# Optimization experiments

Hardware: AMD Instinct MI355X
Metric: run time of the kernel (lower is better)

Reference implementation:

```python
import jax, jax.numpy as jnp
import numpy as np

NBINS = 256


def _equalize_hist(img):
    # img: [H, W] float32 with values in [0, 255]; replicates cv2.equalizeHist
    vals = jnp.clip(img.astype(jnp.int32), 0, NBINS - 1).reshape(-1)
    hist = jnp.zeros((NBINS,), jnp.float32).at[vals].add(1.0)
    cdf = jnp.cumsum(hist)
    total = jnp.float32(vals.shape[0])
    # cdf value at the first nonzero bin (cv2 maps that bin to 0)
    cdf_min = cdf[jnp.argmax(hist > 0)]
    scale = (NBINS - 1.0) / jnp.maximum(total - cdf_min, 1.0)
    lut = jnp.clip(jnp.round((cdf - cdf_min) * scale), 0.0, 255.0)
    return lut[vals].reshape(img.shape) / 255.0


def setup_inputs() -> dict:
    key = jax.random.key(0)
    k1, _ = jax.random.split(key)
    # uint8-like pixel values stored as float32, shape [B, 1, H, W]
    image = jnp.floor(jax.random.uniform(k1, (64, 1, 1024, 1024), jnp.float32) * 256.0)
    image = jnp.clip(image, 0.0, 255.0)
    kernel = jnp.array([[[[0.0, 1.0, 0.0], [1.0, -4.0, 1.0], [0.0, 1.0, 0.0]]]], jnp.float32)
    return {"image": image, "kernel": kernel}


def reference(image, kernel):
    # per-image histogram equalization (channels == 1, as in the torch loop)
    eq = jax.vmap(_equalize_hist)(image[:, 0, :, :])[:, None, :, :]  # [B,1,H,W]
    laplace = jax.lax.conv_general_dilated(
        eq, kernel,
        window_strides=(1, 1), padding=((1, 1), (1, 1)),
        dimension_numbers=("NCHW", "OIHW", "NCHW"))
    # torch.var defaults to unbiased (ddof=1) over all elements
    return jnp.var(laplace, ddof=1)
```

## Files before the change

kernel.cpp:

```cpp
#include <hip/hip_runtime.h>

#define W 1024
#define H 1024
#define NIMG 64
#define NBINS 256
#define NPIX (W * H)
#define NTOT ((long long)NIMG * NPIX)
#define NSLOT 256
#define RPW 8

typedef float f32x4 __attribute__((ext_vector_type(4)));

#define WS_HIST 0
#define WS_LUTP 65536
#define WS_ACC  81920
#define WS_SMALL 86016
#define WS_U8   (128 * 1024)
#define WS_FAST (WS_U8 + (size_t)NIMG * NPIX)

template <bool WRITE_U8>
__global__ __launch_bounds__(256) void hist_kernel(const float* __restrict__ img,
                                                   unsigned int* __restrict__ ghist,
                                                   unsigned char* __restrict__ u8img) {
    __shared__ unsigned int lh[NBINS];
    const int b = blockIdx.y;
    lh[threadIdx.x] = 0u;
    __syncthreads();
    const size_t base = (size_t)b * NPIX;
    const f32x4* p = (const f32x4*)(img + base);
    uchar4* q8 = (uchar4*)(u8img + base);
    const int nvec = NPIX / 4;
    const int stride = gridDim.x * 256;
    for (int i = blockIdx.x * 256 + threadIdx.x; i < nvec; i += stride) {
        f32x4 v = __builtin_nontemporal_load(&p[i]);
        int i0 = min(max((int)v[0], 0), 255);
        int i1 = min(max((int)v[1], 0), 255);
        int i2 = min(max((int)v[2], 0), 255);
        int i3 = min(max((int)v[3], 0), 255);
        atomicAdd(&lh[i0], 1u);
        atomicAdd(&lh[i1], 1u);
        atomicAdd(&lh[i2], 1u);
        atomicAdd(&lh[i3], 1u);
        if (WRITE_U8) {
            q8[i] = make_uchar4((unsigned char)i0, (unsigned char)i1,
                                (unsigned char)i2, (unsigned char)i3);
        }
    }
    __syncthreads();
    unsigned int c = lh[threadIdx.x];
    if (c) atomicAdd(&ghist[b * NBINS + threadIdx.x], c);
}

__global__ __launch_bounds__(256) void lut_kernel(const unsigned int* __restrict__ ghist,
                                                  unsigned int* __restrict__ lutp) {
    __shared__ float cdf[NBINS];
    __shared__ unsigned char lut8[NBINS];
    __shared__ float s_min;
    const int b = blockIdx.x;
    const int t = threadIdx.x;
    cdf[t] = (float)ghist[b * NBINS + t];
    __syncthreads();
    for (int off = 1; off < NBINS; off <<= 1) {
        float add = (t >= off) ? cdf[t - off] : 0.0f;
        __syncthreads();
        cdf[t] += add;
        __syncthreads();
    }
    if (t == 0) {
        float m = 0.0f;
        for (int i = 0; i < NBINS; ++i) {
            if (cdf[i] > 0.0f) { m = cdf[i]; break; }
        }
        s_min = m;
    }
    __syncthreads();
    const float scale = 255.0f / fmaxf((float)NPIX - s_min, 1.0f);
    float L = fminf(fmaxf(rintf((cdf[t] - s_min) * scale), 0.0f), 255.0f);
    lut8[t] = (unsigned char)L;
    __syncthreads();
    if (t < 64) {
        unsigned int w = (unsigned int)lut8[4 * t] |
                         ((unsigned int)lut8[4 * t + 1] << 8) |
                         ((unsigned int)lut8[4 * t + 2] << 16) |
                         ((unsigned int)lut8[4 * t + 3] << 24);
        lutp[b * 64 + t] = w;
    }
}

template <bool USE_U8>
__global__ __launch_bounds__(256) void lap_kernel(const float* __restrict__ img,
                                                  const unsigned char* __restrict__ u8img,
                                                  const unsigned int* __restrict__ lutp,
                                                  unsigned long long* __restrict__ acc) {
    const int b = blockIdx.y;
    const int lane = threadIdx.x & 63;
    const int wv = threadIdx.x >> 6;
    const int y0 = blockIdx.x * (RPW * 4) + wv * RPW;
    const int col0 = lane * 16;
    const unsigned int lutw = lutp[b * 64 + lane];
    const size_t base = (size_t)b * NPIX;
    const unsigned char* rowp8 = u8img + base + col0;
    const float* rowpf = img + base + col0;

    unsigned int p_[4], c_[4], n_[4];

    auto load_raw = [&](int gy, unsigned int raw[4]) {
        if ((unsigned)gy < (unsigned)H) {
            if (USE_U8) {
                uint4 r = *(const uint4*)(rowp8 + (size_t)gy * W);
                raw[0] = r.x; raw[1] = r.y; raw[2] = r.z; raw[3] = r.w;
            } else {
                const f32x4* fp = (const f32x4*)(rowpf + (size_t)gy * W);
#pragma unroll
                for (int k = 0; k < 4; ++k) {
                    f32x4 v = fp[k];
                    unsigned int w = (unsigned int)min(max((int)v[0], 0), 255);
                    w |= (unsigned int)min(max((int)v[1], 0), 255) << 8;
                    w |= (unsigned int)min(max((int)v[2], 0), 255) << 16;
                    w |= (unsigned int)min(max((int)v[3], 0), 255) << 24;
                    raw[k] = w;
                }
            }
        } else {
            raw[0] = raw[1] = raw[2] = raw[3] = 0u;
        }
    };
    auto gather_row = [&](const unsigned int raw[4], bool valid, unsigned int ew[4]) {
#pragma unroll
        for (int k = 0; k < 4; ++k) {
            unsigned int out = 0u;
#pragma unroll
            for (int j = 0; j < 4; ++j) {
                int v = (int)((raw[k] >> (8 * j)) & 0xFFu);
                unsigned int e = (unsigned int)__builtin_amdgcn_ds_bpermute(v & 0xFC, (int)lutw);
                out |= ((e >> ((v & 3) << 3)) & 0xFFu) << (8 * j);
            }
            ew[k] = valid ? out : 0u;
        }
    };

    unsigned int rawB[4], rawC[4];
    load_raw(y0 - 1, rawB);
    gather_row(rawB, y0 - 1 >= 0, p_);
    load_raw(y0, rawB);
    gather_row(rawB, true, c_);
    load_raw(y0 + 1, rawB);

    int s = 0, q = 0;
#pragma unroll
    for (int rr = 0; rr < RPW; ++rr) {
        const int gy = y0 + rr;
        if (rr + 1 < RPW) load_raw(gy + 2, rawC);
        gather_row(rawB, gy + 1 < H, n_);

        unsigned int t3 = (unsigned int)__shfl_up((int)c_[3], 1, 64);
        const int lw = (lane == 0) ? 0 : (int)(t3 >> 24);
        unsigned int t0 = (unsigned int)__shfl_down((int)c_[0], 1, 64);
        const int rw = (lane == 63) ? 0 : (int)(t0 & 0xFFu);

#pragma unroll
        for (int p = 0; p < 16; ++p) {
            const int k = p >> 2, sh = (p & 3) << 3;
            const int c = (int)((c_[k] >> sh) & 0xFFu);
            const int u = (int)((p_[k] >> sh) & 0xFFu);
            const int d = (int)((n_[k] >> sh) & 0xFFu);
            const int l = (p == 0) ? lw
                        : (int)((c_[(p - 1) >> 2] >> (((p - 1) & 3) << 3)) & 0xFFu);
            const int r = (p == 15) ? rw
                        : (int)((c_[(p + 1) >> 2] >> (((p + 1) & 3) << 3)) & 0xFFu);
            const int lap = u + d + l + r - 4 * c;
            s += lap;
            q += lap * lap;
        }
#pragma unroll
        for (int k = 0; k < 4; ++k) { p_[k] = c_[k]; c_[k] = n_[k]; rawB[k] = rawC[k]; }
    }

    long long S = s, Q = q;
    for (int off = 32; off > 0; off >>= 1) {
        S += __shfl_down(S, off, 64);
        Q += __shfl_down(Q, off, 64);
    }
    if (lane == 0) {
        const int wid = (blockIdx.x + blockIdx.y * gridDim.x) * 4 + wv;
        const int slot = wid & (NSLOT - 1);
        atomicAdd(&acc[2 * slot], (unsigned long long)S);
        atomicAdd(&acc[2 * slot + 1], (unsigned long long)Q);
    }
}

__global__ __launch_bounds__(256) void finalize_kernel(const unsigned long long* __restrict__ acc,
                                                       float* __restrict__ out) {
    const int t = threadIdx.x;
    long long S = (long long)acc[2 * t];
    long long Q = (long long)acc[2 * t + 1];
    for (int off = 32; off > 0; off >>= 1) {
        S += __shfl_down(S, off, 64);
        Q += __shfl_down(Q, off, 64);
    }
    __shared__ long long ss[4], sq[4];
    const int wave = t >> 6, lane = t & 63;
    if (lane == 0) { ss[wave] = S; sq[wave] = Q; }
    __syncthreads();
    if (t == 0) {
        long long St = ss[0] + ss[1] + ss[2] + ss[3];
        long long Qt = sq[0] + sq[1] + sq[2] + sq[3];
        const double N = (double)NTOT;
        double Sr = (double)St / 255.0;
        double Qr = (double)Qt / 65025.0;
        out[0] = (float)((Qr - Sr * Sr / N) / (N - 1.0));
    }
}

extern "C" void kernel_launch(void* const* d_in, const int* in_sizes, int n_in,
                              void* d_out, int out_size, void* d_ws, size_t ws_size,
                              hipStream_t stream) {
    const float* img = (const float*)d_in[0];
    float* out = (float*)d_out;

    unsigned int* ghist     = (unsigned int*)((char*)d_ws + WS_HIST);
    unsigned int* lutp      = (unsigned int*)((char*)d_ws + WS_LUTP);
    unsigned long long* acc = (unsigned long long*)((char*)d_ws + WS_ACC);
    unsigned char* u8img    = (unsigned char*)((char*)d_ws + WS_U8);

    const bool fast = (ws_size >= WS_FAST);

    hipMemsetAsync(d_ws, 0, WS_SMALL, stream);

    dim3 hgrid(64, NIMG);
    if (fast) hist_kernel<true><<<hgrid, 256, 0, stream>>>(img, ghist, u8img);
    else      hist_kernel<false><<<hgrid, 256, 0, stream>>>(img, ghist, u8img);

    lut_kernel<<<NIMG, NBINS, 0, stream>>>(ghist, lutp);

    dim3 lgrid(H / (RPW * 4), NIMG);
    if (fast) lap_kernel<true><<<lgrid, 256, 0, stream>>>(img, u8img, lutp, acc);
    else      lap_kernel<false><<<lgrid, 256, 0, stream>>>(img, u8img, lutp, acc);

    finalize_kernel<<<1, 256, 0, stream>>>(acc, out);
}
```

Before: 127.1 us.

## Replace global atomics and memset with partial histograms, LDS LUT gather, per-block sums

The histogram kernel now writes one partial histogram per block, which the LUT kernel sums, and the lap kernel writes per-block partial sums that finalize reduces. This removes the hipMemsetAsync and all global atomics. The LUT is stored as 32-bit entries and read through shared memory instead of a ds_bpermute-packed byte lookup, and rows per wave go from 8 to 16. The float fallback path is dropped, so the code now assumes a large enough workspace, and the 16 unpacked ints per row raise register pressure.

```diff
diff --git a/kernel.cpp b/kernel.cpp
--- a/kernel.cpp
+++ b/kernel.cpp
@@ -6,21 +6,19 @@
 #define NBINS 256
 #define NPIX (W * H)
 #define NTOT ((long long)NIMG * NPIX)
-#define NSLOT 256
-#define RPW 8
+#define HBLK 64
+#define RPW 16
+#define LGRIDX (H / (RPW * 4))
 
 typedef float f32x4 __attribute__((ext_vector_type(4)));
 
-#define WS_HIST 0
-#define WS_LUTP 65536
-#define WS_ACC  81920
-#define WS_SMALL 86016
-#define WS_U8   (128 * 1024)
-#define WS_FAST (WS_U8 + (size_t)NIMG * NPIX)
-
-template <bool WRITE_U8>
+#define WS_PART 0
+#define WS_LUT  (4u * 1024 * 1024)
+#define WS_ACC  (WS_LUT + 64 * 1024)
+#define WS_U8   (8u * 1024 * 1024)
+
 __global__ __launch_bounds__(256) void hist_kernel(const float* __restrict__ img,
-                                                   unsigned int* __restrict__ ghist,
+                                                   unsigned int* __restrict__ part,
                                                    unsigned char* __restrict__ u8img) {
     __shared__ unsigned int lh[NBINS];
     const int b = blockIdx.y;
@@ -41,24 +39,24 @@
         atomicAdd(&lh[i1], 1u);
         atomicAdd(&lh[i2], 1u);
         atomicAdd(&lh[i3], 1u);
-        if (WRITE_U8) {
-            q8[i] = make_uchar4((unsigned char)i0, (unsigned char)i1,
-                                (unsigned char)i2, (unsigned char)i3);
-        }
-    }
-    __syncthreads();
-    unsigned int c = lh[threadIdx.x];
-    if (c) atomicAdd(&ghist[b * NBINS + threadIdx.x], c);
-}
-
-__global__ __launch_bounds__(256) void lut_kernel(const unsigned int* __restrict__ ghist,
-                                                  unsigned int* __restrict__ lutp) {
+        q8[i] = make_uchar4((unsigned char)i0, (unsigned char)i1,
+                            (unsigned char)i2, (unsigned char)i3);
+    }
+    __syncthreads();
+    part[((size_t)b * HBLK + blockIdx.x) * NBINS + threadIdx.x] = lh[threadIdx.x];
+}
+
+__global__ __launch_bounds__(256) void lut_kernel(const unsigned int* __restrict__ part,
+                                                  unsigned int* __restrict__ lut32) {
     __shared__ float cdf[NBINS];
-    __shared__ unsigned char lut8[NBINS];
     __shared__ float s_min;
     const int b = blockIdx.x;
     const int t = threadIdx.x;
-    cdf[t] = (float)ghist[b * NBINS + t];
+    unsigned int h = 0;
+#pragma unroll 8
+    for (int blk = 0; blk < HBLK; ++blk)
+        h += part[((size_t)b * HBLK + blk) * NBINS + t];
+    cdf[t] = (float)h;
     __syncthreads();
     for (int off = 1; off < NBINS; off <<= 1) {
         float add = (t >= off) ? cdf[t - off] : 0.0f;
@@ -76,104 +74,72 @@
     __syncthreads();
     const float scale = 255.0f / fmaxf((float)NPIX - s_min, 1.0f);
     float L = fminf(fmaxf(rintf((cdf[t] - s_min) * scale), 0.0f), 255.0f);
-    lut8[t] = (unsigned char)L;
-    __syncthreads();
-    if (t < 64) {
-        unsigned int w = (unsigned int)lut8[4 * t] |
-                         ((unsigned int)lut8[4 * t + 1] << 8) |
-                         ((unsigned int)lut8[4 * t + 2] << 16) |
-                         ((unsigned int)lut8[4 * t + 3] << 24);
-        lutp[b * 64 + t] = w;
-    }
-}
-
-template <bool USE_U8>
-__global__ __launch_bounds__(256) void lap_kernel(const float* __restrict__ img,
-                                                  const unsigned char* __restrict__ u8img,
-                                                  const unsigned int* __restrict__ lutp,
+    lut32[b * NBINS + t] = (unsigned int)L;
+}
+
+__global__ __launch_bounds__(256) void lap_kernel(const unsigned char* __restrict__ u8img,
+                                                  const unsigned int* __restrict__ lut32,
                                                   unsigned long long* __restrict__ acc) {
+    __shared__ unsigned int slut[NBINS];
     const int b = blockIdx.y;
+    slut[threadIdx.x] = lut32[b * NBINS + threadIdx.x];
+    __syncthreads();
+
     const int lane = threadIdx.x & 63;
     const int wv = threadIdx.x >> 6;
     const int y0 = blockIdx.x * (RPW * 4) + wv * RPW;
-    const int col0 = lane * 16;
-    const unsigned int lutw = lutp[b * 64 + lane];
-    const size_t base = (size_t)b * NPIX;
-    const unsigned char* rowp8 = u8img + base + col0;
-    const float* rowpf = img + base + col0;
-
-    unsigned int p_[4], c_[4], n_[4];
-
-    auto load_raw = [&](int gy, unsigned int raw[4]) {
-        if ((unsigned)gy < (unsigned)H) {
-            if (USE_U8) {
-                uint4 r = *(const uint4*)(rowp8 + (size_t)gy * W);
-                raw[0] = r.x; raw[1] = r.y; raw[2] = r.z; raw[3] = r.w;
-            } else {
-                const f32x4* fp = (const f32x4*)(rowpf + (size_t)gy * W);
-#pragma unroll
-                for (int k = 0; k < 4; ++k) {
-                    f32x4 v = fp[k];
-                    unsigned int w = (unsigned int)min(max((int)v[0], 0), 255);
-                    w |= (unsigned int)min(max((int)v[1], 0), 255) << 8;
-                    w |= (unsigned int)min(max((int)v[2], 0), 255) << 16;
-                    w |= (unsigned int)min(max((int)v[3], 0), 255) << 24;
-                    raw[k] = w;
-                }
-            }
+    const unsigned char* rowp = u8img + (size_t)b * NPIX + lane * 16;
+
+    int pr[16], cr[16], nr[16];
+
+    auto load_raw = [&](int gy, uint4& raw) {
+        if ((unsigned)gy < (unsigned)H) raw = *(const uint4*)(rowp + (size_t)gy * W);
+        else raw = make_uint4(0u, 0u, 0u, 0u);
+    };
+    auto gather = [&](const uint4& raw, bool valid, int out[16]) {
+        const unsigned int w[4] = {raw.x, raw.y, raw.z, raw.w};
+        if (valid) {
+#pragma unroll
+            for (int k = 0; k < 4; ++k)
+#pragma unroll
+                for (int j = 0; j < 4; ++j)
+                    out[4 * k + j] = (int)slut[(w[k] >> (8 * j)) & 0xFFu];
         } else {
-            raw[0] = raw[1] = raw[2] = raw[3] = 0u;
+#pragma unroll
+            for (int p = 0; p < 16; ++p) out[p] = 0;
         }
     };
-    auto gather_row = [&](const unsigned int raw[4], bool valid, unsigned int ew[4]) {
-#pragma unroll
-        for (int k = 0; k < 4; ++k) {
-            unsigned int out = 0u;
-#pragma unroll
-            for (int j = 0; j < 4; ++j) {
-                int v = (int)((raw[k] >> (8 * j)) & 0xFFu);
-                unsigned int e = (unsigned int)__builtin_amdgcn_ds_bpermute(v & 0xFC, (int)lutw);
-                out |= ((e >> ((v & 3) << 3)) & 0xFFu) << (8 * j);
-            }
-            ew[k] = valid ? out : 0u;
-        }
-    };
-
-    unsigned int rawB[4], rawC[4];
-    load_raw(y0 - 1, rawB);
-    gather_row(rawB, y0 - 1 >= 0, p_);
-    load_raw(y0, rawB);
-    gather_row(rawB, true, c_);
-    load_raw(y0 + 1, rawB);
+
+    uint4 rawC, rawN;
+    load_raw(y0 - 1, rawC);
+    gather(rawC, y0 - 1 >= 0, pr);
+    load_raw(y0, rawC);
+    gather(rawC, true, cr);
+    load_raw(y0 + 1, rawC);
 
     int s = 0, q = 0;
 #pragma unroll
     for (int rr = 0; rr < RPW; ++rr) {
         const int gy = y0 + rr;
-        if (rr + 1 < RPW) load_raw(gy + 2, rawC);
-        gather_row(rawB, gy + 1 < H, n_);
-
-        unsigned int t3 = (unsigned int)__shfl_up((int)c_[3], 1, 64);
-        const int lw = (lane == 0) ? 0 : (int)(t3 >> 24);
-        unsigned int t0 = (unsigned int)__shfl_down((int)c_[0], 1, 64);
-        const int rw = (lane == 63) ? 0 : (int)(t0 & 0xFFu);
+        load_raw(gy + 2, rawN);
+        gather(rawC, gy + 1 < H, nr);
+
+        int lw = __shfl_up(cr[15], 1, 64);
+        lw = (lane == 0) ? 0 : lw;
+        int rw = __shfl_down(cr[0], 1, 64);
+        rw = (lane == 63) ? 0 : rw;
 
 #pragma unroll
         for (int p = 0; p < 16; ++p) {
-            const int k = p >> 2, sh = (p & 3) << 3;
-            const int c = (int)((c_[k] >> sh) & 0xFFu);
-            const int u = (int)((p_[k] >> sh) & 0xFFu);
-            const int d = (int)((n_[k] >> sh) & 0xFFu);
-            const int l = (p == 0) ? lw
-                        : (int)((c_[(p - 1) >> 2] >> (((p - 1) & 3) << 3)) & 0xFFu);
-            const int r = (p == 15) ? rw
-                        : (int)((c_[(p + 1) >> 2] >> (((p + 1) & 3) << 3)) & 0xFFu);
-            const int lap = u + d + l + r - 4 * c;
+            const int l = (p == 0) ? lw : cr[p - 1];
+            const int r = (p == 15) ? rw : cr[p + 1];
+            const int lap = pr[p] + nr[p] + l + r - 4 * cr[p];
             s += lap;
             q += lap * lap;
         }
 #pragma unroll
-        for (int k = 0; k < 4; ++k) { p_[k] = c_[k]; c_[k] = n_[k]; rawB[k] = rawC[k]; }
+        for (int p = 0; p < 16; ++p) { pr[p] = cr[p]; cr[p] = nr[p]; }
+        rawC = rawN;
     }
 
     long long S = s, Q = q;
@@ -181,19 +147,27 @@
         S += __shfl_down(S, off, 64);
         Q += __shfl_down(Q, off, 64);
     }
-    if (lane == 0) {
-        const int wid = (blockIdx.x + blockIdx.y * gridDim.x) * 4 + wv;
-        const int slot = wid & (NSLOT - 1);
-        atomicAdd(&acc[2 * slot], (unsigned long long)S);
-        atomicAdd(&acc[2 * slot + 1], (unsigned long long)Q);
+    __shared__ long long ss[4], sq[4];
+    if (lane == 0) { ss[wv] = S; sq[wv] = Q; }
+    __syncthreads();
+    if (threadIdx.x == 0) {
+        long long St = ss[0] + ss[1] + ss[2] + ss[3];
+        long long Qt = sq[0] + sq[1] + sq[2] + sq[3];
+        const int blk = blockIdx.x + blockIdx.y * gridDim.x;
+        acc[2 * blk]     = (unsigned long long)St;
+        acc[2 * blk + 1] = (unsigned long long)Qt;
     }
 }
 
 __global__ __launch_bounds__(256) void finalize_kernel(const unsigned long long* __restrict__ acc,
                                                        float* __restrict__ out) {
     const int t = threadIdx.x;
-    long long S = (long long)acc[2 * t];
-    long long Q = (long long)acc[2 * t + 1];
+    long long S = 0, Q = 0;
+#pragma unroll
+    for (int i = 0; i < NIMG * LGRIDX; i += 256) {
+        S += (long long)acc[2 * (i + t)];
+        Q += (long long)acc[2 * (i + t) + 1];
+    }
     for (int off = 32; off > 0; off >>= 1) {
         S += __shfl_down(S, off, 64);
         Q += __shfl_down(Q, off, 64);
@@ -218,24 +192,18 @@
     const float* img = (const float*)d_in[0];
     float* out = (float*)d_out;
 
-    unsigned int* ghist     = (unsigned int*)((char*)d_ws + WS_HIST);
-    unsigned int* lutp      = (unsigned int*)((char*)d_ws + WS_LUTP);
+    unsigned int* part      = (unsigned int*)((char*)d_ws + WS_PART);
+    unsigned int* lut32     = (unsigned int*)((char*)d_ws + WS_LUT);
     unsigned long long* acc = (unsigned long long*)((char*)d_ws + WS_ACC);
     unsigned char* u8img    = (unsigned char*)((char*)d_ws + WS_U8);
 
-    const bool fast = (ws_size >= WS_FAST);
-
-    hipMemsetAsync(d_ws, 0, WS_SMALL, stream);
-
-    dim3 hgrid(64, NIMG);
-    if (fast) hist_kernel<true><<<hgrid, 256, 0, stream>>>(img, ghist, u8img);
-    else      hist_kernel<false><<<hgrid, 256, 0, stream>>>(img, ghist, u8img);
-
-    lut_kernel<<<NIMG, NBINS, 0, stream>>>(ghist, lutp);
-
-    dim3 lgrid(H / (RPW * 4), NIMG);
-    if (fast) lap_kernel<true><<<lgrid, 256, 0, stream>>>(img, u8img, lutp, acc);
-    else      lap_kernel<false><<<lgrid, 256, 0, stream>>>(img, u8img, lutp, acc);
+    dim3 hgrid(HBLK, NIMG);
+    hist_kernel<<<hgrid, 256, 0, stream>>>(img, part, u8img);
+
+    lut_kernel<<<NIMG, NBINS, 0, stream>>>(part, lut32);
+
+    dim3 lgrid(LGRIDX, NIMG);
+    lap_kernel<<<lgrid, 256, 0, stream>>>(u8img, lut32, acc);
 
     finalize_kernel<<<1, 256, 0, stream>>>(acc, out);
 }
```

Result: no change. 129.2 us (+1.6%).
